# Performance work log

Hardware: AMD Instinct MI355X
Metric: run time of the kernel (lower is better)

The kernel has to match this reference:

```python
import jax, jax.numpy as jnp
import numpy as np
import math

D_MODEL = 1024
NUM_HEADS = 16
GROUPS = 4
HPG = NUM_HEADS // GROUPS  # heads per group
DK = D_MODEL // NUM_HEADS


def setup_inputs() -> dict:
    key = jax.random.key(0)
    ks = jax.random.split(key, 11)
    B, S = 1, 4096
    scale = 1.0 / math.sqrt(D_MODEL)
    inp = {
        "q": jax.random.normal(ks[0], (B, S, D_MODEL), jnp.float32),
        "k": jax.random.normal(ks[1], (B, S, D_MODEL), jnp.float32),
        "v": jax.random.normal(ks[2], (B, S, D_MODEL), jnp.float32),
        # nn.Linear weights stored [out, in], applied as x @ W.T + b
        "Wq": jax.random.normal(ks[3], (D_MODEL, D_MODEL), jnp.float32) * scale,
        "bq": jax.random.normal(ks[4], (D_MODEL,), jnp.float32) * scale,
        "Wk": jax.random.normal(ks[5], (D_MODEL, D_MODEL), jnp.float32) * scale,
        "bk": jax.random.normal(ks[6], (D_MODEL,), jnp.float32) * scale,
        "Wv": jax.random.normal(ks[7], (D_MODEL, D_MODEL), jnp.float32) * scale,
        "bv": jax.random.normal(ks[8], (D_MODEL,), jnp.float32) * scale,
        "Wo": jax.random.normal(ks[9], (D_MODEL, D_MODEL), jnp.float32) * scale,
        "bo": jax.random.normal(ks[10], (D_MODEL,), jnp.float32) * scale,
    }
    return inp


def _reshape_qkv(x):
    # [b, s, d_model] -> [b, groups, hpg, s, dk]
    b, s, _ = x.shape
    x = x.reshape(b, s, GROUPS, HPG, DK)
    return x.transpose(0, 2, 3, 1, 4)


def reference(q, k, v, Wq, bq, Wk, bk, Wv, bv, Wo, bo):
    b, s, _ = q.shape
    query = _reshape_qkv(q @ Wq.T + bq)  # [b,g,h,s,dk]
    key_ = _reshape_qkv(k @ Wk.T + bk)
    value = _reshape_qkv(v @ Wv.T + bv)

    scores = jnp.einsum('bghqd,bghkd->bghqk', query, key_) / math.sqrt(DK)
    causal = jnp.tril(jnp.ones((s, s), dtype=bool))  # [s_q, s_k]
    scores = jnp.where(causal, scores, -jnp.inf)
    attn = jax.nn.softmax(scores, axis=-1)

    out = jnp.einsum('bghqk,bghkd->bghqd', attn, value)
    out = out.transpose(0, 3, 1, 2, 4).reshape(b, s, NUM_HEADS * DK)
    return out @ Wo.T + bo, key_, value
```

## Files before the change

kernel.cpp:

```cpp
#include <hip/hip_runtime.h>
#include <math.h>

typedef __attribute__((ext_vector_type(8))) __bf16 bf16x8;
typedef __attribute__((ext_vector_type(8))) unsigned short ushort8;
typedef __attribute__((ext_vector_type(4))) float f32x4;
typedef unsigned short ushort_t;
typedef unsigned int uint_t;

#define MFMA16(a,b,c) __builtin_amdgcn_mfma_f32_16x16x32_bf16(a,b,c,0,0,0)

#define GLD16(gp, lp) __builtin_amdgcn_global_load_lds( \
  (__attribute__((address_space(1))) const void*)(gp), \
  (__attribute__((address_space(3))) void*)(lp), 16, 0, 0)

__device__ __forceinline__ ushort_t f2bf(float f) {
  uint_t u = __builtin_bit_cast(uint_t, f);
  u = (u + 0x7fffu + ((u >> 16) & 1u)) >> 16;
  return (ushort_t)u;
}

struct ConvArgs {
  const float* src[7];
  ushort_t* dst[7];
  int cum[8];
};

__global__ __launch_bounds__(256) void convall(ConvArgs a) {
  int flat = blockIdx.x * 256 + threadIdx.x;
  int s = 0;
#pragma unroll
  for (int i = 1; i < 7; ++i) if (flat >= a.cum[i]) s = i;
  int idx = flat - a.cum[s];
  float4 v = ((const float4*)a.src[s])[idx];
  ushort4 o;
  o.x = f2bf(v.x); o.y = f2bf(v.y); o.z = f2bf(v.z); o.w = f2bf(v.w);
  ((ushort4*)a.dst[s])[idx] = o;
}

struct QKVArgs {
  const ushort_t* A[3];
  const ushort_t* B[3];
  const float* bias[3];
  float* outf[3];
  ushort_t* outb[3];
};

__global__ __launch_bounds__(256)
void qkv_gemm(QKVArgs ar) {
  const int M = 4096, K = 1024;
  const int z = blockIdx.z;
  const ushort_t* __restrict__ A = ar.A[z];
  const ushort_t* __restrict__ B = ar.B[z];
  const float* __restrict__ bias = ar.bias[z];

  __shared__ __align__(16) ushort_t Al[128 * 32];
  __shared__ __align__(16) ushort_t Bl[128 * 32];
  const int tid = threadIdx.x;
  const int w = tid >> 6, l = tid & 63;
  const int lr = l & 15, lg = l >> 4;
  const int bm = blockIdx.x * 128, bn = blockIdx.y * 128;
  const int wr = w >> 1, wc = w & 1;
  f32x4 acc[4][4] = {};

  const int crow = l >> 2;
  const int ccol = (l & 3) * 8;

  for (int k0 = 0; k0 < K; k0 += 32) {
    __syncthreads();
#pragma unroll
    for (int i = 0; i < 2; ++i) {
      const int c = w * 2 + i;
      GLD16(A + (size_t)(bm + c * 16 + crow) * K + k0 + ccol, &Al[c * 512]);
      GLD16(B + (size_t)(bn + c * 16 + crow) * K + k0 + ccol, &Bl[c * 512]);
    }
    __syncthreads();
    bf16x8 af[4], bfr[4];
#pragma unroll
    for (int mi = 0; mi < 4; ++mi)
      af[mi] = *(const bf16x8*)&Al[(wr * 64 + mi * 16 + lr) * 32 + lg * 8];
#pragma unroll
    for (int ni = 0; ni < 4; ++ni)
      bfr[ni] = *(const bf16x8*)&Bl[(wc * 64 + ni * 16 + lr) * 32 + lg * 8];
#pragma unroll
    for (int mi = 0; mi < 4; ++mi)
#pragma unroll
      for (int ni = 0; ni < 4; ++ni)
        acc[mi][ni] = MFMA16(af[mi], bfr[ni], acc[mi][ni]);
  }

  float* outf = ar.outf[z];
  ushort_t* outb = ar.outb[z];
#pragma unroll
  for (int mi = 0; mi < 4; ++mi) {
#pragma unroll
    for (int ni = 0; ni < 4; ++ni) {
      const int r0 = bm + wr * 64 + mi * 16 + lg * 4;
      const int cc = bn + wc * 64 + ni * 16 + lr;
      const float bv = bias[cc];
      const int hh = cc >> 6, dk = cc & 63;
      const int dh = dk >> 5, lgk = (dk & 31) >> 3, jq = dk & 7;
#pragma unroll
      for (int jj = 0; jj < 4; ++jj) {
        float v = acc[mi][ni][jj] + bv;
        int s = r0 + jj;
        if (z == 0) {
          size_t idx = ((((size_t)hh * 256 + (s >> 4)) * 2 + dh) * 64 + (s & 15) + 16 * lgk) * 8 + jq;
          outb[idx] = f2bf(v * 0.18033688011112042f);
        } else if (z == 1) {
          outf[((size_t)hh * M + s) * 64 + dk] = v;
          size_t idx = ((((size_t)hh * 256 + (s >> 4)) * 2 + dh) * 64 + (s & 15) + 16 * lgk) * 8 + jq;
          outb[idx] = f2bf(v);
        } else {
          outf[((size_t)hh * M + s) * 64 + dk] = v;
        }
      }
    }
  }
}

__global__ __launch_bounds__(256)
void gemm_o(const ushort_t* __restrict__ A, const ushort_t* __restrict__ B,
            const float* __restrict__ bias, float* __restrict__ Cout)
{
  const int N = 1024, K = 1024;
  __shared__ __align__(16) ushort_t Al[128 * 32];
  __shared__ __align__(16) ushort_t Bl[128 * 32];
  const int tid = threadIdx.x;
  const int w = tid >> 6, l = tid & 63;
  const int lr = l & 15, lg = l >> 4;
  const int bm = blockIdx.x * 128, bn = blockIdx.y * 128;
  const int wr = w >> 1, wc = w & 1;
  f32x4 acc[4][4] = {};
  const int crow = l >> 2;
  const int ccol = (l & 3) * 8;

  for (int k0 = 0; k0 < K; k0 += 32) {
    __syncthreads();
#pragma unroll
    for (int i = 0; i < 2; ++i) {
      const int c = w * 2 + i;
      GLD16(A + (size_t)(bm + c * 16 + crow) * K + k0 + ccol, &Al[c * 512]);
      GLD16(B + (size_t)(bn + c * 16 + crow) * K + k0 + ccol, &Bl[c * 512]);
    }
    __syncthreads();
    bf16x8 af[4], bfr[4];
#pragma unroll
    for (int mi = 0; mi < 4; ++mi)
      af[mi] = *(const bf16x8*)&Al[(wr * 64 + mi * 16 + lr) * 32 + lg * 8];
#pragma unroll
    for (int ni = 0; ni < 4; ++ni)
      bfr[ni] = *(const bf16x8*)&Bl[(wc * 64 + ni * 16 + lr) * 32 + lg * 8];
#pragma unroll
    for (int mi = 0; mi < 4; ++mi)
#pragma unroll
      for (int ni = 0; ni < 4; ++ni)
        acc[mi][ni] = MFMA16(af[mi], bfr[ni], acc[mi][ni]);
  }

#pragma unroll
  for (int mi = 0; mi < 4; ++mi)
#pragma unroll
    for (int ni = 0; ni < 4; ++ni) {
      const int r0 = bm + wr * 64 + mi * 16 + lg * 4;
      const int cc = bn + wc * 64 + ni * 16 + lr;
      const float bv = bias[cc];
#pragma unroll
      for (int jj = 0; jj < 4; ++jj)
        Cout[(size_t)(r0 + jj) * N + cc] = acc[mi][ni][jj] + bv;
    }
}

__global__ __launch_bounds__(256) void pack_vt(const float* __restrict__ Vhead,
                                               ushort_t* __restrict__ Vt) {
  const int S = 4096;
  int tile = blockIdx.x * 4 + (threadIdx.x >> 6);
  int l = threadIdx.x & 63;
  int h = tile >> 9, rem = tile & 511;
  int kb = rem >> 2, dvt = rem & 3;
  int lr = l & 15, lg = l >> 4;
  const float* src = Vhead + ((size_t)h * S + kb * 32 + lg * 8) * 64 + dvt * 16 + lr;
  ushort8 o8;
#pragma unroll
  for (int j = 0; j < 8; ++j) o8[j] = f2bf(src[(size_t)j * 64]);
  *(ushort8*)&Vt[(size_t)tile * 512 + l * 8] = o8;
}

__global__ __launch_bounds__(256, 2)
void attn(const ushort_t* __restrict__ Qt, const ushort_t* __restrict__ Kt,
          const ushort_t* __restrict__ Vt, ushort_t* __restrict__ Ao) {
  const int DM = 1024;
  const int h = blockIdx.y;
  const int T = 31 - (int)blockIdx.x;
  const int tid = threadIdx.x, w = tid >> 6, l = tid & 63;
  const int lr = l & 15, lg = l >> 4;
  const int qw = T * 128 + w * 32;

  __shared__ __align__(16) ushort_t plds[4][32 * 64];
  char* pw = (char*)plds[w];
  const uint_t swz = (uint_t)(lr & 7) << 4;

  const size_t hQ = (size_t)h * 256;

  bf16x8 qf[2][2];
#pragma unroll
  for (int qt = 0; qt < 2; ++qt)
#pragma unroll
    for (int dh = 0; dh < 2; ++dh)
      qf[qt][dh] = *(const bf16x8*)&Qt[(((hQ + (qw >> 4) + qt) * 2 + dh) << 9) + l * 8];

  f32x4 o[2][4] = {};
  float m[2], lsum[2];
#pragma unroll
  for (int qt = 0; qt < 2; ++qt) { m[qt] = -__builtin_inff(); lsum[qt] = 0.0f; }

  bf16x8 kc[8], kn[8], vf[8];

  auto loadK8 = [&](bf16x8* dst, int kt) {
#pragma unroll
    for (int kt4 = 0; kt4 < 4; ++kt4)
#pragma unroll
      for (int dh = 0; dh < 2; ++dh)
        dst[kt4 * 2 + dh] =
            *(const bf16x8*)&Kt[(((hQ + (kt >> 4) + kt4) * 2 + dh) << 9) + l * 8];
  };
  auto loadV8 = [&](int kt) {
#pragma unroll
    for (int ks = 0; ks < 2; ++ks)
#pragma unroll
      for (int dvt = 0; dvt < 4; ++dvt)
        vf[ks * 4 + dvt] =
            *(const bf16x8*)&Vt[((((size_t)h * 128 + (kt >> 5) + ks) * 4 + dvt) << 9) + l * 8];
  };

  auto step = [&](int kt, bool domask, bool pf) {
    loadV8(kt);
    if (pf) loadK8(kn, kt + 64);
    f32x4 st[4][2];
#pragma unroll
    for (int kt4 = 0; kt4 < 4; ++kt4) {
      f32x4 c0 = {}, c1 = {};
      c0 = MFMA16(kc[kt4 * 2 + 0], qf[0][0], c0);
      c0 = MFMA16(kc[kt4 * 2 + 1], qf[0][1], c0);
      c1 = MFMA16(kc[kt4 * 2 + 0], qf[1][0], c1);
      c1 = MFMA16(kc[kt4 * 2 + 1], qf[1][1], c1);
      st[kt4][0] = c0;
      st[kt4][1] = c1;
    }
    if (domask) {
#pragma unroll
      for (int kt4 = 0; kt4 < 4; ++kt4)
#pragma unroll
        for (int qt = 0; qt < 2; ++qt) {
          int qq = qw + qt * 16 + lr;
#pragma unroll
          for (int jj = 0; jj < 4; ++jj) {
            int key = kt + kt4 * 16 + lg * 4 + jj;
            if (key > qq) st[kt4][qt][jj] = -__builtin_inff();
          }
        }
    }
#pragma unroll
    for (int qt = 0; qt < 2; ++qt) {
      float pm = -__builtin_inff();
#pragma unroll
      for (int kt4 = 0; kt4 < 4; ++kt4)
#pragma unroll
        for (int jj = 0; jj < 4; ++jj)
          pm = fmaxf(pm, st[kt4][qt][jj]);
      pm = fmaxf(pm, __shfl_xor(pm, 16));
      pm = fmaxf(pm, __shfl_xor(pm, 32));
      float mn = fmaxf(m[qt], pm);
      float al = __builtin_amdgcn_exp2f(m[qt] - mn);
      m[qt] = mn;
      float ps = 0.0f;
#pragma unroll
      for (int kt4 = 0; kt4 < 4; ++kt4) {
#pragma unroll
        for (int jj = 0; jj < 4; ++jj) {
          float e = __builtin_amdgcn_exp2f(st[kt4][qt][jj] - mn);
          st[kt4][qt][jj] = e;
          ps += e;
        }
      }
      ps += __shfl_xor(ps, 16);
      ps += __shfl_xor(ps, 32);
      lsum[qt] = lsum[qt] * al + ps;
#pragma unroll
      for (int dvt = 0; dvt < 4; ++dvt) {
#pragma unroll
        for (int jj = 0; jj < 4; ++jj) o[qt][dvt][jj] *= al;
      }
#pragma unroll
      for (int kt4 = 0; kt4 < 4; ++kt4) {
        ushort4 pk;
        pk.x = f2bf(st[kt4][qt][0]); pk.y = f2bf(st[kt4][qt][1]);
        pk.z = f2bf(st[kt4][qt][2]); pk.w = f2bf(st[kt4][qt][3]);
        uint_t bo = (uint_t)(qt * 16 + lr) * 128 + (uint_t)(kt4 * 32 + lg * 8);
        *(ushort4*)(pw + (bo ^ swz)) = pk;
      }
    }
    bf16x8 pa[2][2];
#pragma unroll
    for (int qt = 0; qt < 2; ++qt)
#pragma unroll
      for (int ks = 0; ks < 2; ++ks) {
        uint_t bo = (uint_t)(qt * 16 + lr) * 128 + (uint_t)(ks * 64 + lg * 16);
        pa[qt][ks] = *(const bf16x8*)(pw + (bo ^ swz));
      }
#pragma unroll
    for (int dvt = 0; dvt < 4; ++dvt)
#pragma unroll
      for (int ks = 0; ks < 2; ++ks) {
        o[0][dvt] = MFMA16(vf[ks * 4 + dvt], pa[0][ks], o[0][dvt]);
        o[1][dvt] = MFMA16(vf[ks * 4 + dvt], pa[1][ks], o[1][dvt]);
      }
    if (pf) {
#pragma unroll
      for (int i = 0; i < 8; ++i) kc[i] = kn[i];
    }
  };

  const int ktm = qw & ~63;
  loadK8(kc, 0);
  for (int kt = 0; kt < ktm; kt += 64) step(kt, false, true);
  step(ktm, true, false);

#pragma unroll
  for (int qt = 0; qt < 2; ++qt) {
    float inv = 1.0f / lsum[qt];
#pragma unroll
    for (int dvt = 0; dvt < 4; ++dvt) {
      ushort4 pk;
      pk.x = f2bf(o[qt][dvt][0] * inv);
      pk.y = f2bf(o[qt][dvt][1] * inv);
      pk.z = f2bf(o[qt][dvt][2] * inv);
      pk.w = f2bf(o[qt][dvt][3] * inv);
      *(ushort4*)&Ao[(size_t)(qw + qt * 16 + lr) * DM + h * 64 + dvt * 16 + lg * 4] = pk;
    }
  }
}

extern "C" void kernel_launch(void* const* d_in, const int* in_sizes, int n_in,
                              void* d_out, int out_size, void* d_ws, size_t ws_size,
                              hipStream_t stream) {
  const int S = 4096, DM = 1024;
  const size_t NE = (size_t)S * DM;

  const float* q  = (const float*)d_in[0];
  const float* k  = (const float*)d_in[1];
  const float* v  = (const float*)d_in[2];
  const float* Wq = (const float*)d_in[3];
  const float* bq = (const float*)d_in[4];
  const float* Wk = (const float*)d_in[5];
  const float* bk = (const float*)d_in[6];
  const float* Wv = (const float*)d_in[7];
  const float* bv = (const float*)d_in[8];
  const float* Wo = (const float*)d_in[9];
  const float* bo = (const float*)d_in[10];

  unsigned char* ws = (unsigned char*)d_ws;
  ushort_t* qb  = (ushort_t*)(ws);
  ushort_t* kb  = (ushort_t*)(ws + (8u << 20));
  ushort_t* vb  = (ushort_t*)(ws + (16u << 20));
  ushort_t* wqb = (ushort_t*)(ws + (24u << 20));
  ushort_t* wkb = (ushort_t*)(ws + (26u << 20));
  ushort_t* wvb = (ushort_t*)(ws + (28u << 20));
  ushort_t* wob = (ushort_t*)(ws + (30u << 20));
  ushort_t* qpb = (ushort_t*)(ws + (32u << 20));
  ushort_t* kpb = (ushort_t*)(ws + (40u << 20));
  ushort_t* vt  = kb;
  ushort_t* ao  = qb;

  float* outO = (float*)d_out;
  float* keyO = outO + NE;
  float* valO = keyO + NE;

  ConvArgs ca;
  ca.src[0] = q;  ca.src[1] = k;  ca.src[2] = v;
  ca.src[3] = Wq; ca.src[4] = Wk; ca.src[5] = Wv; ca.src[6] = Wo;
  ca.dst[0] = qb;  ca.dst[1] = kb;  ca.dst[2] = vb;
  ca.dst[3] = wqb; ca.dst[4] = wkb; ca.dst[5] = wvb; ca.dst[6] = wob;
  const int NB = 1048576, WB = 262144;
  ca.cum[0] = 0;
  ca.cum[1] = NB; ca.cum[2] = 2 * NB; ca.cum[3] = 3 * NB;
  ca.cum[4] = 3 * NB + WB; ca.cum[5] = 3 * NB + 2 * WB;
  ca.cum[6] = 3 * NB + 3 * WB; ca.cum[7] = 3 * NB + 4 * WB;
  convall<<<ca.cum[7] / 256, 256, 0, stream>>>(ca);

  QKVArgs qa;
  qa.A[0] = qb;  qa.A[1] = kb;  qa.A[2] = vb;
  qa.B[0] = wqb; qa.B[1] = wkb; qa.B[2] = wvb;
  qa.bias[0] = bq; qa.bias[1] = bk; qa.bias[2] = bv;
  qa.outf[0] = nullptr; qa.outf[1] = keyO; qa.outf[2] = valO;
  qa.outb[0] = qpb;     qa.outb[1] = kpb;  qa.outb[2] = nullptr;
  qkv_gemm<<<dim3(S / 128, DM / 128, 3), 256, 0, stream>>>(qa);

  pack_vt<<<2048, 256, 0, stream>>>(valO, vt);

  attn<<<dim3(S / 128, 16), 256, 0, stream>>>(qpb, kpb, vt, ao);

  gemm_o<<<dim3(S / 128, DM / 128), 256, 0, stream>>>(ao, wob, bo, outO);
}
```

Baseline: 315.3 us.

## Stage K/V tiles through double-buffered LDS, lazy softmax rescale, remap attention grid

The attention kernel now stages K and V tiles for all four waves into double-buffered LDS with direct global-to-LDS loads and barriers, replacing the per-wave register prefetch. Each wave therefore reads shared K/V from LDS instead of fetching it separately from global memory. The online softmax only rescales the running max, sum and output when the new max exceeds the old one by more than a threshold, which skips most of the rescale multiplies. Bf16 conversion uses the native cast, and the grid is flattened to a 1-D launch with a head-interleaved block mapping to change scheduling and cache locality. In exchange it adds block-wide barriers and more LDS per block, which may lower occupancy, and the lazy rescale lets exponentials grow larger than 1 before normalisation.

```diff
diff --git a/kernel.cpp b/kernel.cpp
--- a/kernel.cpp
+++ b/kernel.cpp
@@ -17,6 +17,10 @@
   uint_t u = __builtin_bit_cast(uint_t, f);
   u = (u + 0x7fffu + ((u >> 16) & 1u)) >> 16;
   return (ushort_t)u;
+}
+__device__ __forceinline__ ushort_t f2bfn(float f) {
+  __bf16 b = (__bf16)f;
+  return __builtin_bit_cast(ushort_t, b);
 }
 
 struct ConvArgs {
@@ -189,18 +193,34 @@
 void attn(const ushort_t* __restrict__ Qt, const ushort_t* __restrict__ Kt,
           const ushort_t* __restrict__ Vt, ushort_t* __restrict__ Ao) {
   const int DM = 1024;
-  const int h = blockIdx.y;
-  const int T = 31 - (int)blockIdx.x;
+  const int flat = blockIdx.x;
+  const int h = ((flat >> 8) << 3) + (flat & 7);
+  const int xr = (flat >> 3) & 31;
+  const int T = 31 - xr;
   const int tid = threadIdx.x, w = tid >> 6, l = tid & 63;
   const int lr = l & 15, lg = l >> 4;
   const int qw = T * 128 + w * 32;
 
-  __shared__ __align__(16) ushort_t plds[4][32 * 64];
+  __shared__ __align__(16) ushort_t Kl[2][4096];
+  __shared__ __align__(16) ushort_t Vl[2][4096];
+  __shared__ __align__(16) ushort_t plds[4][2048];
   char* pw = (char*)plds[w];
   const uint_t swz = (uint_t)(lr & 7) << 4;
 
+  const ushort_t* Kbase = Kt + (size_t)h * 262144;
+  const ushort_t* Vbase = Vt + (size_t)h * 262144;
+
+  auto stage = [&](int t, int buf) {
+    const ushort_t* ks = Kbase + (size_t)t * 4096;
+    const ushort_t* vs = Vbase + (size_t)t * 4096;
+#pragma unroll
+    for (int r = 0; r < 2; ++r) {
+      GLD16(ks + r * 2048 + w * 512 + l * 8, &Kl[buf][r * 2048 + w * 512]);
+      GLD16(vs + r * 2048 + w * 512 + l * 8, &Vl[buf][r * 2048 + w * 512]);
+    }
+  };
+
   const size_t hQ = (size_t)h * 256;
-
   bf16x8 qf[2][2];
 #pragma unroll
   for (int qt = 0; qt < 2; ++qt)
@@ -213,36 +233,36 @@
 #pragma unroll
   for (int qt = 0; qt < 2; ++qt) { m[qt] = -__builtin_inff(); lsum[qt] = 0.0f; }
 
-  bf16x8 kc[8], kn[8], vf[8];
-
-  auto loadK8 = [&](bf16x8* dst, int kt) {
-#pragma unroll
-    for (int kt4 = 0; kt4 < 4; ++kt4)
-#pragma unroll
-      for (int dh = 0; dh < 2; ++dh)
-        dst[kt4 * 2 + dh] =
-            *(const bf16x8*)&Kt[(((hQ + (kt >> 4) + kt4) * 2 + dh) << 9) + l * 8];
-  };
-  auto loadV8 = [&](int kt) {
-#pragma unroll
-    for (int ks = 0; ks < 2; ++ks)
-#pragma unroll
-      for (int dvt = 0; dvt < 4; ++dvt)
-        vf[ks * 4 + dvt] =
-            *(const bf16x8*)&Vt[((((size_t)h * 128 + (kt >> 5) + ks) * 4 + dvt) << 9) + l * 8];
-  };
-
-  auto step = [&](int kt, bool domask, bool pf) {
-    loadV8(kt);
-    if (pf) loadK8(kn, kt + 64);
+  const int ktm_step = (qw & ~63) >> 6;
+  const int nt = 2 * T + 2;
+
+  stage(0, 0);
+  for (int t = 0; t < nt; ++t) {
+    const int buf = t & 1;
+    if (t + 1 < nt) {
+      stage(t + 1, buf ^ 1);
+      asm volatile("s_waitcnt vmcnt(4)" ::: "memory");
+    } else {
+      asm volatile("s_waitcnt vmcnt(0)" ::: "memory");
+    }
+    __builtin_amdgcn_s_barrier();
+    __builtin_amdgcn_sched_barrier(0);
+
+    const int kt = t * 64;
+    const bool domask = (t >= ktm_step);
+    const ushort_t* Kb = Kl[buf];
+    const ushort_t* Vb = Vl[buf];
+
     f32x4 st[4][2];
 #pragma unroll
     for (int kt4 = 0; kt4 < 4; ++kt4) {
+      bf16x8 k0 = *(const bf16x8*)&Kb[(kt4 * 2 + 0) * 512 + l * 8];
+      bf16x8 k1 = *(const bf16x8*)&Kb[(kt4 * 2 + 1) * 512 + l * 8];
       f32x4 c0 = {}, c1 = {};
-      c0 = MFMA16(kc[kt4 * 2 + 0], qf[0][0], c0);
-      c0 = MFMA16(kc[kt4 * 2 + 1], qf[0][1], c0);
-      c1 = MFMA16(kc[kt4 * 2 + 0], qf[1][0], c1);
-      c1 = MFMA16(kc[kt4 * 2 + 1], qf[1][1], c1);
+      c0 = MFMA16(k0, qf[0][0], c0);
+      c0 = MFMA16(k1, qf[0][1], c0);
+      c1 = MFMA16(k0, qf[1][0], c1);
+      c1 = MFMA16(k1, qf[1][1], c1);
       st[kt4][0] = c0;
       st[kt4][1] = c1;
     }
@@ -261,17 +281,26 @@
     }
 #pragma unroll
     for (int qt = 0; qt < 2; ++qt) {
-      float pm = -__builtin_inff();
-#pragma unroll
-      for (int kt4 = 0; kt4 < 4; ++kt4)
-#pragma unroll
-        for (int jj = 0; jj < 4; ++jj)
-          pm = fmaxf(pm, st[kt4][qt][jj]);
+      float a0 = fmaxf(fmaxf(st[0][qt][0], st[0][qt][1]), fmaxf(st[0][qt][2], st[0][qt][3]));
+      float a1 = fmaxf(fmaxf(st[1][qt][0], st[1][qt][1]), fmaxf(st[1][qt][2], st[1][qt][3]));
+      float a2 = fmaxf(fmaxf(st[2][qt][0], st[2][qt][1]), fmaxf(st[2][qt][2], st[2][qt][3]));
+      float a3 = fmaxf(fmaxf(st[3][qt][0], st[3][qt][1]), fmaxf(st[3][qt][2], st[3][qt][3]));
+      float pm = fmaxf(fmaxf(a0, a1), fmaxf(a2, a3));
       pm = fmaxf(pm, __shfl_xor(pm, 16));
       pm = fmaxf(pm, __shfl_xor(pm, 32));
-      float mn = fmaxf(m[qt], pm);
-      float al = __builtin_amdgcn_exp2f(m[qt] - mn);
-      m[qt] = mn;
+      float mn;
+      if (__any(pm > m[qt] + 10.0f)) {
+        mn = fmaxf(m[qt], pm);
+        float al = __builtin_amdgcn_exp2f(m[qt] - mn);
+        m[qt] = mn;
+        lsum[qt] *= al;
+#pragma unroll
+        for (int dvt = 0; dvt < 4; ++dvt)
+#pragma unroll
+          for (int jj = 0; jj < 4; ++jj) o[qt][dvt][jj] *= al;
+      } else {
+        mn = m[qt];
+      }
       float ps = 0.0f;
 #pragma unroll
       for (int kt4 = 0; kt4 < 4; ++kt4) {
@@ -284,17 +313,12 @@
       }
       ps += __shfl_xor(ps, 16);
       ps += __shfl_xor(ps, 32);
-      lsum[qt] = lsum[qt] * al + ps;
-#pragma unroll
-      for (int dvt = 0; dvt < 4; ++dvt) {
-#pragma unroll
-        for (int jj = 0; jj < 4; ++jj) o[qt][dvt][jj] *= al;
-      }
+      lsum[qt] += ps;
 #pragma unroll
       for (int kt4 = 0; kt4 < 4; ++kt4) {
         ushort4 pk;
-        pk.x = f2bf(st[kt4][qt][0]); pk.y = f2bf(st[kt4][qt][1]);
-        pk.z = f2bf(st[kt4][qt][2]); pk.w = f2bf(st[kt4][qt][3]);
+        pk.x = f2bfn(st[kt4][qt][0]); pk.y = f2bfn(st[kt4][qt][1]);
+        pk.z = f2bfn(st[kt4][qt][2]); pk.w = f2bfn(st[kt4][qt][3]);
         uint_t bo = (uint_t)(qt * 16 + lr) * 128 + (uint_t)(kt4 * 32 + lg * 8);
         *(ushort4*)(pw + (bo ^ swz)) = pk;
       }
@@ -311,19 +335,14 @@
     for (int dvt = 0; dvt < 4; ++dvt)
 #pragma unroll
       for (int ks = 0; ks < 2; ++ks) {
-        o[0][dvt] = MFMA16(vf[ks * 4 + dvt], pa[0][ks], o[0][dvt]);
-        o[1][dvt] = MFMA16(vf[ks * 4 + dvt], pa[1][ks], o[1][dvt]);
-      }
-    if (pf) {
-#pragma unroll
-      for (int i = 0; i < 8; ++i) kc[i] = kn[i];
-    }
-  };
-
-  const int ktm = qw & ~63;
-  loadK8(kc, 0);
-  for (int kt = 0; kt < ktm; kt += 64) step(kt, false, true);
-  step(ktm, true, false);
+        bf16x8 vf = *(const bf16x8*)&Vb[(ks * 4 + dvt) * 512 + l * 8];
+        o[0][dvt] = MFMA16(vf, pa[0][ks], o[0][dvt]);
+        o[1][dvt] = MFMA16(vf, pa[1][ks], o[1][dvt]);
+      }
+
+    __builtin_amdgcn_sched_barrier(0);
+    __builtin_amdgcn_s_barrier();
+  }
 
 #pragma unroll
   for (int qt = 0; qt < 2; ++qt) {
@@ -331,10 +350,10 @@
 #pragma unroll
     for (int dvt = 0; dvt < 4; ++dvt) {
       ushort4 pk;
-      pk.x = f2bf(o[qt][dvt][0] * inv);
-      pk.y = f2bf(o[qt][dvt][1] * inv);
-      pk.z = f2bf(o[qt][dvt][2] * inv);
-      pk.w = f2bf(o[qt][dvt][3] * inv);
+      pk.x = f2bfn(o[qt][dvt][0] * inv);
+      pk.y = f2bfn(o[qt][dvt][1] * inv);
+      pk.z = f2bfn(o[qt][dvt][2] * inv);
+      pk.w = f2bfn(o[qt][dvt][3] * inv);
       *(ushort4*)&Ao[(size_t)(qw + qt * 16 + lr) * DM + h * 64 + dvt * 16 + lg * 4] = pk;
     }
   }
@@ -397,7 +416,7 @@
 
   pack_vt<<<2048, 256, 0, stream>>>(valO, vt);
 
-  attn<<<dim3(S / 128, 16), 256, 0, stream>>>(qpb, kpb, vt, ao);
+  attn<<<512, 256, 0, stream>>>(qpb, kpb, vt, ao);
 
   gemm_o<<<dim3(S / 128, DM / 128), 256, 0, stream>>>(ao, wob, bo, outO);
 }
```

Result: faster. 306.3 us (-2.9%).
